# Performance work log

Measured on AMD Instinct MI355X. Metric: run time of the kernel, lower is better.

Reference implementation:

```python
import jax, jax.numpy as jnp
import numpy as np

N = 65536      # n query/support points
NN = 34        # neighbors per point
K = 15         # kernel points
IN_F = 64
OUT_F = 64
RADIUS = 2.5
KP_EXTENT_CFG = 1.0
DENSITY = 5.0
EXTENT = KP_EXTENT_CFG * RADIUS / DENSITY  # effective KP_extent = 0.5
BN_EPS = 1e-6
LRELU_SLOPE = 0.1
POINT_DIM = 4  # modulated=True -> 3 offset dims + 1 modulation per kernel point


def make_kernel_points():
    # Deterministic stand-in for the precomputed kernel dispositions loaded
    # from disk in KPConv (fixed='center': first point at origin). Points lie
    # inside a ball of radius 1.5 * extent.
    rng = np.random.RandomState(42)
    kp = rng.normal(size=(K, 3))
    kp /= np.linalg.norm(kp, axis=1, keepdims=True)
    kp *= rng.uniform(0.3, 1.0, size=(K, 1))
    kp[0] = 0.0
    return jnp.asarray(kp * (1.5 * EXTENT), dtype=jnp.float32)


def setup_inputs() -> dict:
    key = jax.random.key(0)
    ks = jax.random.split(key, 8)
    query_points = jax.random.uniform(ks[0], (N, 3), dtype=jnp.float32)
    support_points = jax.random.uniform(ks[1], (N, 3), dtype=jnp.float32)
    neighbors_indices = jax.random.randint(ks[2], (N, NN), 0, N, dtype=jnp.int32)
    features = jax.random.normal(ks[3], (N, IN_F), dtype=jnp.float32)
    # weight_variable: truncated normal with std sqrt(2/size[-1])
    weight = jax.random.truncated_normal(ks[4], -2.0, 2.0, (K, IN_F, OUT_F), jnp.float32) * np.sqrt(2.0 / OUT_F)
    off_dim = POINT_DIM * K
    offset_weight = jax.random.truncated_normal(ks[5], -2.0, 2.0, (K, IN_F, off_dim), jnp.float32) * np.sqrt(2.0 / off_dim)
    offset_bias = jnp.zeros((off_dim,), jnp.float32)
    bn_gamma = jnp.ones((OUT_F,), jnp.float32)
    bn_beta = jnp.zeros((OUT_F,), jnp.float32)
    kernel_points = make_kernel_points()
    return dict(query_points=query_points, support_points=support_points,
                neighbors_indices=neighbors_indices, features=features,
                weight=weight, offset_weight=offset_weight, offset_bias=offset_bias,
                bn_gamma=bn_gamma, bn_beta=bn_beta, kernel_points=kernel_points)


def _influence(sq_dist):
    # KP_influence='linear': relu(1 - d / extent)
    return jax.nn.relu(1.0 - jnp.sqrt(sq_dist) / EXTENT)


def reference(query_points, support_points, neighbors_indices, features,
              weight, offset_weight, offset_bias, bn_gamma, bn_beta, kernel_points):
    n = query_points.shape[0]
    # Shadow point (far away) / shadow feature (zeros) appended at index n0
    supp_pad = jnp.concatenate([support_points, jnp.full((1, 3), 1e6, jnp.float32)], 0)
    feat_pad = jnp.concatenate([features, jnp.zeros((1, IN_F), jnp.float32)], 0)

    neigh_pts = supp_pad[neighbors_indices] - query_points[:, None, :]   # [n,nn,3]
    neigh_feats = feat_pad[neighbors_indices]                            # [n,nn,in]

    # ---- rigid KPConv producing per-point offsets (+ modulations) ----
    sq0 = jnp.sum((neigh_pts[:, :, None, :] - kernel_points[None, None]) ** 2, -1)  # [n,nn,K]
    w0 = _influence(sq0)
    wf0 = jnp.einsum('nak,nac->nkc', w0, neigh_feats)                    # [n,K,in]
    f0 = jnp.einsum('nkc,kcd->nd', wf0, offset_weight) + offset_bias     # [n,4K]
    offsets = f0[:, :3 * K].reshape(n, K, 3) * EXTENT                    # rescale to layer extent
    modulations = 2.0 * jax.nn.sigmoid(f0[:, 3 * K:])                    # [n,K]

    # ---- deformable KPConv ----
    def_kp = kernel_points[None] + offsets                               # [n,K,3]
    sq = jnp.sum((neigh_pts[:, :, None, :] - def_kp[:, None, :, :]) ** 2, -1)  # [n,nn,K]
    w = _influence(sq)                                                   # aggregation_mode='sum'
    wf = jnp.einsum('nak,nac->nkc', w, neigh_feats) * modulations[:, :, None]
    x = jnp.einsum('nkc,kco->no', wf, weight)                            # [n,out]

    # BatchNorm1d (training-mode batch stats, eps=1e-6) + LeakyReLU(0.1)
    mean = x.mean(0)
    var = x.var(0)
    x = (x - mean) * jax.lax.rsqrt(var + BN_EPS) * bn_gamma + bn_beta
    return jnp.where(x >= 0, x, LRELU_SLOPE * x)
```

## Files before the change

### kernel.cpp

```cpp
#include <hip/hip_runtime.h>
#include <math.h>

#define NPTS 65536

using half8   = __attribute__((ext_vector_type(8))) _Float16;
using half4   = __attribute__((ext_vector_type(4))) _Float16;
using floatx4 = __attribute__((ext_vector_type(4))) float;

__global__ __launch_bounds__(256) void k_prep(
    const float* __restrict__ ow, const float* __restrict__ w,
    const float* __restrict__ feat,
    _Float16* __restrict__ owt, _Float16* __restrict__ wt,
    _Float16* __restrict__ featH, float* __restrict__ stats)
{
  int b = blockIdx.x;
  if (b < 256) {
    int i = b * 256 + threadIdx.x;
    int d = i >> 10, kc = i & 1023, c = kc >> 4, k = kc & 15;
    owt[i] = (k < 15 && d < 60) ? (_Float16)ow[(k * 64 + c) * 60 + d] : (_Float16)0.f;
    wt[i]  = (k < 15) ? (_Float16)w[(k * 64 + c) * 64 + d] : (_Float16)0.f;
    if (b == 0 && threadIdx.x < 128) stats[threadIdx.x] = 0.f;
  } else {
    int j = (b - 256) * 256 + threadIdx.x;
    float4 f = ((const float4*)feat)[j];
    half4 h = {(_Float16)f.x, (_Float16)f.y, (_Float16)f.z, (_Float16)f.w};
    ((half4*)featH)[j] = h;
  }
}

__global__ __launch_bounds__(256, 4) void k_fused(
    const float* __restrict__ query, const float* __restrict__ support,
    const int* __restrict__ nidx, const _Float16* __restrict__ featH,
    const float* __restrict__ kpts, const float* __restrict__ obias,
    const _Float16* __restrict__ owt, const _Float16* __restrict__ wt,
    float* __restrict__ outx, float* __restrict__ stats)
{
  __shared__ float4                 np4[16][34];
  __shared__ unsigned short         sidx[16][34];
  __shared__ __align__(16) _Float16 fT[4][64 * 32];
  __shared__ unsigned int           fx2[4][64];
  __shared__ __align__(16) _Float16 wfh[16 * 264];
  __shared__ float                  dk[16][60];

  const int tid  = threadIdx.x;
  const int wave = tid >> 6, lane = tid & 63;
  const int quad = lane >> 4, mm = lane & 15;
  const int base = blockIdx.x * 16;
  _Float16* fTw = fT[wave];
  unsigned int* fTw32 = (unsigned int*)fTw;
  unsigned int* fx2w = fx2[wave];
  const floatx4 fz = {0.f, 0.f, 0.f, 0.f};
  const int me = (mm < 15) ? mm : 14;

  for (int s = tid; s < 544; s += 256) {
    int pt = s / 34, a = s - pt * 34;
    int n = base + pt;
    int id = nidx[n * 34 + a];
    float dx = support[id * 3 + 0] - query[n * 3 + 0];
    float dy = support[id * 3 + 1] - query[n * 3 + 1];
    float dz = support[id * 3 + 2] - query[n * 3 + 2];
    float4 q = {dx, dy, dz, dx * dx + dy * dy + dz * dz};
    np4[pt][a] = q;
    sidx[pt][a] = (unsigned short)id;
  }
  __syncthreads();

  auto load_g = [&](int pl, uint4* g0, uint4* g1) {
    #pragma unroll
    for (int it = 0; it < 3; ++it) {
      int task = it * 64 + lane;
      if (task < 136) {
        int rp = task >> 3, ch = task & 7;
        int i0 = (int)sidx[pl][2 * rp], i1 = (int)sidx[pl][2 * rp + 1];
        g0[it] = *(const uint4*)(featH + i0 * 64 + ch * 8);
        g1[it] = *(const uint4*)(featH + i1 * 64 + ch * 8);
      }
    }
  };
  auto transpose_g = [&](const uint4* g0, const uint4* g1) {
    #pragma unroll
    for (int it = 0; it < 3; ++it) {
      int task = it * 64 + lane;
      if (task < 136) {
        int rp = task >> 3, ch = task & 7;
        const uint* p0 = (const uint*)&g0[it];
        const uint* p1 = (const uint*)&g1[it];
        if (rp < 16) {
          int chunk = rp >> 2, o = rp & 3;
          #pragma unroll
          for (int cc = 0; cc < 8; ++cc) {
            int c  = ch * 8 + cc;
            int pc = chunk ^ ((ch ^ cc) & 3);
            uint v = __builtin_amdgcn_perm(p1[cc >> 1], p0[cc >> 1],
                                           (cc & 1) ? 0x07060302u : 0x05040100u);
            fTw32[c * 16 + pc * 4 + o] = v;
          }
        } else {
          #pragma unroll
          for (int cc = 0; cc < 8; ++cc) {
            uint v = __builtin_amdgcn_perm(p1[cc >> 1], p0[cc >> 1],
                                           (cc & 1) ? 0x07060302u : 0x05040100u);
            fx2w[ch * 8 + cc] = v;
          }
        }
      }
    }
  };

  auto conv_point = [&](int pl, float kx, float ky, float kz, float modme,
                        half4* hq) {
    float hk = kx * kx + ky * ky + kz * kz;
    half8 a0;
    #pragma unroll
    for (int j = 0; j < 8; ++j) {
      int a = quad * 8 + j;
      float4 q = np4[pl][a];
      float dt = q.x * kx + q.y * ky + q.z * kz;
      float d2 = fmaxf(q.w + hk - 2.f * dt, 0.f);
      a0[j] = (_Float16)(fmaxf(1.f - 2.f * sqrtf(d2), 0.f) * modme);
    }
    float4 q = np4[pl][32];
    float dt = q.x * kx + q.y * ky + q.z * kz;
    float w32 = fmaxf(1.f - 2.f * sqrtf(fmaxf(q.w + hk - 2.f * dt, 0.f)), 0.f) * modme;
    q = np4[pl][33];
    dt = q.x * kx + q.y * ky + q.z * kz;
    float w33 = fmaxf(1.f - 2.f * sqrtf(fmaxf(q.w + hk - 2.f * dt, 0.f)), 0.f) * modme;
    half8 a2 = {};
    a2[0] = (_Float16)((quad == 0) ? w32 : 0.f);
    a2[1] = (_Float16)((quad == 0) ? w33 : 0.f);
    #pragma unroll
    for (int ct = 0; ct < 4; ++ct) {
      int c  = ct * 16 + mm;
      int pc = quad ^ (((c >> 3) ^ c) & 3);
      half8 b = *(const half8*)(fTw + c * 32 + pc * 8);
      floatx4 acc = __builtin_amdgcn_mfma_f32_16x16x32_f16(a0, b, fz, 0, 0, 0);
      uint fp = fx2w[c];
      half8 b2 = {};
      b2[0] = __builtin_bit_cast(_Float16, (unsigned short)(fp & 0xffffu));
      b2[1] = __builtin_bit_cast(_Float16, (unsigned short)(fp >> 16));
      acc = __builtin_amdgcn_mfma_f32_16x16x32_f16(a2, b2, acc, 0, 0, 0);
      half4 h = {(_Float16)acc[0], (_Float16)acc[1],
                 (_Float16)acc[2], (_Float16)acc[3]};
      if (ct == 0) *(half4*)(wfh + pl * 264 + mm * 16 + quad * 4) = h;
      else         hq[ct - 1] = h;
    }
  };

  auto write_hold = [&](const half4 (*hq)[3], int idx) {
    #pragma unroll
    for (int pp = 0; pp < 4; ++pp)
      *(half4*)(wfh + (wave * 4 + pp) * 264 + mm * 16 + quad * 4) = hq[pp][idx];
  };

  auto gemm_q = [&](const _Float16* bmat, int p, floatx4& A, floatx4& B) {
    const _Float16* brow = bmat + (wave * 16 + mm) * 1024 + p * 256;
    const _Float16* arow = wfh + mm * 264;
    #pragma unroll
    for (int k2 = 0; k2 < 8; ++k2) {
      half8 af = *(const half8*)(arow + k2 * 32 + quad * 8);
      half8 bf = *(const half8*)(brow + k2 * 32 + quad * 8);
      if (k2 & 1) B = __builtin_amdgcn_mfma_f32_16x16x32_f16(af, bf, B, 0, 0, 0);
      else        A = __builtin_amdgcn_mfma_f32_16x16x32_f16(af, bf, A, 0, 0, 0);
    }
  };

  uint4 G0[2][3], G1[2][3];
  half4 hq[4][3];
  const float k0x = kpts[me * 3 + 0], k0y = kpts[me * 3 + 1], k0z = kpts[me * 3 + 2];

  {
    load_g(wave * 4, G0[0], G1[0]);
    #pragma unroll
    for (int pp = 0; pp < 4; ++pp) {
      int pl = wave * 4 + pp;
      if (pp < 3) load_g(pl + 1, G0[(pp + 1) & 1], G1[(pp + 1) & 1]);
      transpose_g(G0[pp & 1], G1[pp & 1]);
      conv_point(pl, k0x, k0y, k0z, 1.f, hq[pp]);
    }
  }
  load_g(wave * 4, G0[0], G1[0]);
  __syncthreads();

  {
    floatx4 A = fz, B = fz;
    gemm_q(owt, 0, A, B);
    __syncthreads(); write_hold(hq, 0); __syncthreads();
    gemm_q(owt, 1, A, B);
    __syncthreads(); write_hold(hq, 1); __syncthreads();
    gemm_q(owt, 2, A, B);
    __syncthreads(); write_hold(hq, 2); __syncthreads();
    gemm_q(owt, 3, A, B);
    int d = wave * 16 + mm;
    float bv = (d < 60) ? obias[d] : 0.f;
    float kv = (d < 45) ? kpts[d] : 0.f;
    #pragma unroll
    for (int r = 0; r < 4; ++r) {
      int pt = quad * 4 + r;
      float v = A[r] + B[r] + bv;
      if (d < 60)
        dk[pt][d] = (d < 45) ? (kv + 0.5f * v)
                             : (2.f / (1.f + expf(-v)));
    }
  }
  __syncthreads();

  #pragma unroll
  for (int pp = 0; pp < 4; ++pp) {
    int pl = wave * 4 + pp;
    if (pp < 3) load_g(pl + 1, G0[(pp + 1) & 1], G1[(pp + 1) & 1]);
    float kx = dk[pl][me * 3 + 0], ky = dk[pl][me * 3 + 1], kz = dk[pl][me * 3 + 2];
    float modme = dk[pl][45 + me];
    transpose_g(G0[pp & 1], G1[pp & 1]);
    conv_point(pl, kx, ky, kz, modme, hq[pp]);
  }
  __syncthreads();

  {
    floatx4 A = fz, B = fz;
    gemm_q(wt, 0, A, B);
    __syncthreads(); write_hold(hq, 0); __syncthreads();
    gemm_q(wt, 1, A, B);
    __syncthreads(); write_hold(hq, 1); __syncthreads();
    gemm_q(wt, 2, A, B);
    __syncthreads(); write_hold(hq, 2); __syncthreads();
    gemm_q(wt, 3, A, B);
    int d = wave * 16 + mm;
    float s1 = 0.f, s2 = 0.f;
    #pragma unroll
    for (int r = 0; r < 4; ++r) {
      float v = A[r] + B[r];
      outx[(base + quad * 4 + r) * 64 + d] = v;
      s1 += v; s2 += v * v;
    }
    s1 += __shfl_xor(s1, 16); s2 += __shfl_xor(s2, 16);
    s1 += __shfl_xor(s1, 32); s2 += __shfl_xor(s2, 32);
    if (lane < 16) {
      atomicAdd(&stats[d], s1);
      atomicAdd(&stats[64 + d], s2);
    }
  }
}

__global__ __launch_bounds__(256) void k_norm(
    float* __restrict__ x, const float* __restrict__ stats,
    const float* __restrict__ gamma, const float* __restrict__ beta)
{
  const int i = blockIdx.x * 256 + threadIdx.x;
  float4 v = ((float4*)x)[i];
  const int c0 = (i * 4) & 63;
  float o[4] = {v.x, v.y, v.z, v.w};
  #pragma unroll
  for (int j = 0; j < 4; ++j) {
    int c = c0 + j;
    float mean = stats[c] * (1.f / NPTS);
    float var  = stats[64 + c] * (1.f / NPTS) - mean * mean;
    float s = rsqrtf(var + 1e-6f) * gamma[c];
    float y = (o[j] - mean) * s + beta[c];
    o[j] = (y >= 0.f) ? y : 0.1f * y;
  }
  float4 rv = {o[0], o[1], o[2], o[3]};
  ((float4*)x)[i] = rv;
}

extern "C" void kernel_launch(void* const* d_in, const int* in_sizes, int n_in,
                              void* d_out, int out_size, void* d_ws, size_t ws_size,
                              hipStream_t stream)
{
  const float* query   = (const float*)d_in[0];
  const float* support = (const float*)d_in[1];
  const int*   nidx    = (const int*)d_in[2];
  const float* feat    = (const float*)d_in[3];
  const float* weight  = (const float*)d_in[4];
  const float* oweight = (const float*)d_in[5];
  const float* obias   = (const float*)d_in[6];
  const float* gamma   = (const float*)d_in[7];
  const float* beta    = (const float*)d_in[8];
  const float* kpts    = (const float*)d_in[9];
  float* x = (float*)d_out;

  char* ws = (char*)d_ws;
  _Float16* featH = (_Float16*)ws;
  _Float16* owt   = (_Float16*)(ws + 8388608);
  _Float16* wt    = (_Float16*)(ws + 8519680);
  float*    stats = (float*)(ws + 8650752);

  k_prep<<<4352, 256, 0, stream>>>(oweight, weight, feat, owt, wt, featH, stats);
  k_fused<<<4096, 256, 0, stream>>>(query, support, nidx, featH, kpts, obias,
                                    owt, wt, x, stats);
  k_norm<<<4096, 256, 0, stream>>>(x, stats, gamma, beta);
}
```

Baseline: 310.7 us.

## Stage WF in halves and gather tail-neighbor features once per block

Doubles the shared WF staging buffer so each channel-wise GEMM runs in two halves instead of four quarters. This cuts the barrier/write-hold rounds from three to one per GEMM and reduces the per-wave register hold from three to two half4 tiles. The features of the last two neighbors (32,33) are now gathered and transposed once per block into a per-point shared array, which removes the irregular 136-task loop and its branches from each wave's load/transpose. In exchange, LDS use grows and launch bounds drop occupancy from 4 to 3 blocks per CU.

```diff
diff --git a/kernel.cpp b/kernel.cpp
--- a/kernel.cpp
+++ b/kernel.cpp
@@ -28,7 +28,7 @@
   }
 }
 
-__global__ __launch_bounds__(256, 4) void k_fused(
+__global__ __launch_bounds__(256, 3) void k_fused(
     const float* __restrict__ query, const float* __restrict__ support,
     const int* __restrict__ nidx, const _Float16* __restrict__ featH,
     const float* __restrict__ kpts, const float* __restrict__ obias,
@@ -38,8 +38,8 @@
   __shared__ float4                 np4[16][34];
   __shared__ unsigned short         sidx[16][34];
   __shared__ __align__(16) _Float16 fT[4][64 * 32];
-  __shared__ unsigned int           fx2[4][64];
-  __shared__ __align__(16) _Float16 wfh[16 * 264];
+  __shared__ unsigned int           fx2s[16][64];
+  __shared__ __align__(16) _Float16 wfh[16 * 520];
   __shared__ float                  dk[16][60];
 
   const int tid  = threadIdx.x;
@@ -48,7 +48,6 @@
   const int base = blockIdx.x * 16;
   _Float16* fTw = fT[wave];
   unsigned int* fTw32 = (unsigned int*)fTw;
-  unsigned int* fx2w = fx2[wave];
   const floatx4 fz = {0.f, 0.f, 0.f, 0.f};
   const int me = (mm < 15) ? mm : 14;
 
@@ -65,50 +64,53 @@
   }
   __syncthreads();
 
+  if (tid < 128) {
+    int pt = tid >> 3, ch = tid & 7;
+    int i0 = (int)sidx[pt][32], i1 = (int)sidx[pt][33];
+    uint4 g0 = *(const uint4*)(featH + i0 * 64 + ch * 8);
+    uint4 g1 = *(const uint4*)(featH + i1 * 64 + ch * 8);
+    const uint* p0 = (const uint*)&g0;
+    const uint* p1 = (const uint*)&g1;
+    #pragma unroll
+    for (int cc = 0; cc < 8; ++cc) {
+      uint v = __builtin_amdgcn_perm(p1[cc >> 1], p0[cc >> 1],
+                                     (cc & 1) ? 0x07060302u : 0x05040100u);
+      fx2s[pt][ch * 8 + cc] = v;
+    }
+  }
+  __syncthreads();
+
   auto load_g = [&](int pl, uint4* g0, uint4* g1) {
     #pragma unroll
-    for (int it = 0; it < 3; ++it) {
+    for (int it = 0; it < 2; ++it) {
       int task = it * 64 + lane;
-      if (task < 136) {
-        int rp = task >> 3, ch = task & 7;
-        int i0 = (int)sidx[pl][2 * rp], i1 = (int)sidx[pl][2 * rp + 1];
-        g0[it] = *(const uint4*)(featH + i0 * 64 + ch * 8);
-        g1[it] = *(const uint4*)(featH + i1 * 64 + ch * 8);
+      int rp = task >> 3, ch = task & 7;
+      int i0 = (int)sidx[pl][2 * rp], i1 = (int)sidx[pl][2 * rp + 1];
+      g0[it] = *(const uint4*)(featH + i0 * 64 + ch * 8);
+      g1[it] = *(const uint4*)(featH + i1 * 64 + ch * 8);
+    }
+  };
+  auto transpose_g = [&](const uint4* g0, const uint4* g1) {
+    #pragma unroll
+    for (int it = 0; it < 2; ++it) {
+      int task = it * 64 + lane;
+      int rp = task >> 3, ch = task & 7;
+      int chunk = rp >> 2, o = rp & 3;
+      const uint* p0 = (const uint*)&g0[it];
+      const uint* p1 = (const uint*)&g1[it];
+      #pragma unroll
+      for (int cc = 0; cc < 8; ++cc) {
+        int c  = ch * 8 + cc;
+        int pc = chunk ^ ((ch ^ cc) & 3);
+        uint v = __builtin_amdgcn_perm(p1[cc >> 1], p0[cc >> 1],
+                                       (cc & 1) ? 0x07060302u : 0x05040100u);
+        fTw32[c * 16 + pc * 4 + o] = v;
       }
     }
   };
-  auto transpose_g = [&](const uint4* g0, const uint4* g1) {
-    #pragma unroll
-    for (int it = 0; it < 3; ++it) {
-      int task = it * 64 + lane;
-      if (task < 136) {
-        int rp = task >> 3, ch = task & 7;
-        const uint* p0 = (const uint*)&g0[it];
-        const uint* p1 = (const uint*)&g1[it];
-        if (rp < 16) {
-          int chunk = rp >> 2, o = rp & 3;
-          #pragma unroll
-          for (int cc = 0; cc < 8; ++cc) {
-            int c  = ch * 8 + cc;
-            int pc = chunk ^ ((ch ^ cc) & 3);
-            uint v = __builtin_amdgcn_perm(p1[cc >> 1], p0[cc >> 1],
-                                           (cc & 1) ? 0x07060302u : 0x05040100u);
-            fTw32[c * 16 + pc * 4 + o] = v;
-          }
-        } else {
-          #pragma unroll
-          for (int cc = 0; cc < 8; ++cc) {
-            uint v = __builtin_amdgcn_perm(p1[cc >> 1], p0[cc >> 1],
-                                           (cc & 1) ? 0x07060302u : 0x05040100u);
-            fx2w[ch * 8 + cc] = v;
-          }
-        }
-      }
-    }
-  };
 
   auto conv_point = [&](int pl, float kx, float ky, float kz, float modme,
-                        half4* hq) {
+                        half4* hq2) {
     float hk = kx * kx + ky * ky + kz * kz;
     half8 a0;
     #pragma unroll
@@ -134,29 +136,33 @@
       int pc = quad ^ (((c >> 3) ^ c) & 3);
       half8 b = *(const half8*)(fTw + c * 32 + pc * 8);
       floatx4 acc = __builtin_amdgcn_mfma_f32_16x16x32_f16(a0, b, fz, 0, 0, 0);
-      uint fp = fx2w[c];
+      uint fp = fx2s[pl][c];
       half8 b2 = {};
       b2[0] = __builtin_bit_cast(_Float16, (unsigned short)(fp & 0xffffu));
       b2[1] = __builtin_bit_cast(_Float16, (unsigned short)(fp >> 16));
       acc = __builtin_amdgcn_mfma_f32_16x16x32_f16(a2, b2, acc, 0, 0, 0);
       half4 h = {(_Float16)acc[0], (_Float16)acc[1],
                  (_Float16)acc[2], (_Float16)acc[3]};
-      if (ct == 0) *(half4*)(wfh + pl * 264 + mm * 16 + quad * 4) = h;
-      else         hq[ct - 1] = h;
-    }
-  };
-
-  auto write_hold = [&](const half4 (*hq)[3], int idx) {
-    #pragma unroll
-    for (int pp = 0; pp < 4; ++pp)
-      *(half4*)(wfh + (wave * 4 + pp) * 264 + mm * 16 + quad * 4) = hq[pp][idx];
-  };
-
-  auto gemm_q = [&](const _Float16* bmat, int p, floatx4& A, floatx4& B) {
-    const _Float16* brow = bmat + (wave * 16 + mm) * 1024 + p * 256;
-    const _Float16* arow = wfh + mm * 264;
-    #pragma unroll
-    for (int k2 = 0; k2 < 8; ++k2) {
+      if (ct < 2) *(half4*)(wfh + pl * 520 + (ct * 16 + mm) * 16 + quad * 4) = h;
+      else        hq2[ct - 2] = h;
+    }
+  };
+
+  auto write_hold = [&](const half4 (*hq)[2]) {
+    #pragma unroll
+    for (int pp = 0; pp < 4; ++pp) {
+      #pragma unroll
+      for (int t = 0; t < 2; ++t)
+        *(half4*)(wfh + (wave * 4 + pp) * 520 + (t * 16 + mm) * 16 + quad * 4) =
+            hq[pp][t];
+    }
+  };
+
+  auto gemm_half = [&](const _Float16* bmat, int koff, floatx4& A, floatx4& B) {
+    const _Float16* brow = bmat + (wave * 16 + mm) * 1024 + koff;
+    const _Float16* arow = wfh + mm * 520;
+    #pragma unroll
+    for (int k2 = 0; k2 < 16; ++k2) {
       half8 af = *(const half8*)(arow + k2 * 32 + quad * 8);
       half8 bf = *(const half8*)(brow + k2 * 32 + quad * 8);
       if (k2 & 1) B = __builtin_amdgcn_mfma_f32_16x16x32_f16(af, bf, B, 0, 0, 0);
@@ -164,8 +170,8 @@
     }
   };
 
-  uint4 G0[2][3], G1[2][3];
-  half4 hq[4][3];
+  uint4 G0[2][2], G1[2][2];
+  half4 hq[4][2];
   const float k0x = kpts[me * 3 + 0], k0y = kpts[me * 3 + 1], k0z = kpts[me * 3 + 2];
 
   {
@@ -183,13 +189,11 @@
 
   {
     floatx4 A = fz, B = fz;
-    gemm_q(owt, 0, A, B);
-    __syncthreads(); write_hold(hq, 0); __syncthreads();
-    gemm_q(owt, 1, A, B);
-    __syncthreads(); write_hold(hq, 1); __syncthreads();
-    gemm_q(owt, 2, A, B);
-    __syncthreads(); write_hold(hq, 2); __syncthreads();
-    gemm_q(owt, 3, A, B);
+    gemm_half(owt, 0, A, B);
+    __syncthreads();
+    write_hold(hq);
+    __syncthreads();
+    gemm_half(owt, 512, A, B);
     int d = wave * 16 + mm;
     float bv = (d < 60) ? obias[d] : 0.f;
     float kv = (d < 45) ? kpts[d] : 0.f;
@@ -217,13 +221,11 @@
 
   {
     floatx4 A = fz, B = fz;
-    gemm_q(wt, 0, A, B);
-    __syncthreads(); write_hold(hq, 0); __syncthreads();
-    gemm_q(wt, 1, A, B);
-    __syncthreads(); write_hold(hq, 1); __syncthreads();
-    gemm_q(wt, 2, A, B);
-    __syncthreads(); write_hold(hq, 2); __syncthreads();
-    gemm_q(wt, 3, A, B);
+    gemm_half(wt, 0, A, B);
+    __syncthreads();
+    write_hold(hq);
+    __syncthreads();
+    gemm_half(wt, 512, A, B);
     int d = wave * 16 + mm;
     float s1 = 0.f, s2 = 0.f;
     #pragma unroll
```

Measured after the change: 290.4 us. 6.5% less time.
